# Kernel optimization log

Measured on AMD Instinct MI355X. Metric: run time of the kernel, lower is better.

The kernel has to match this reference:

```python
import jax, jax.numpy as jnp
import numpy as np

R, M, A = 512, 256, 256
B, L = 64, 4096


def setup_inputs() -> dict:
    key = jax.random.key(0)
    k1, k2, k3, k4, k5 = jax.random.split(key, 5)
    return {
        "hidden_state": jax.random.normal(k1, (B, R), dtype=jnp.float32),
        "feature_vectors": jax.random.normal(k2, (B, L, M), dtype=jnp.float32),
        "Wa": jax.random.normal(k3, (A, R), dtype=jnp.float32) / np.sqrt(R),
        "Ua": jax.random.normal(k4, (A, M), dtype=jnp.float32) / np.sqrt(M),
        "w": jax.random.normal(k5, (A, 1), dtype=jnp.float32),
        "ba": jnp.zeros((1, A), dtype=jnp.float32),
    }


def reference(hidden_state, feature_vectors, Wa, Ua, w, ba):
    # q: [B, A] broadcast over L; k: [B, L, A]
    q = hidden_state @ Wa.T + ba                      # [B, A]
    k = jnp.einsum("blm,am->bla", feature_vectors, Ua)  # [B, L, A]
    e = jnp.tanh(q[:, None, :] + k) @ w               # [B, L, 1]
    attn = jax.nn.softmax(e, axis=1)                  # softmax over L
    context = jnp.sum(attn * feature_vectors, axis=1)  # [B, M]
    return context
```

## Files before the change

kernel.cpp:

```cpp
#include <hip/hip_runtime.h>
#include <hip/hip_bf16.h>

#define B_  64
#define R_  512
#define M_  256
#define A_  256
#define L_  4096

typedef float    f32x4 __attribute__((ext_vector_type(4)));
typedef _Float16 f16x8 __attribute__((ext_vector_type(8)));

__global__ __launch_bounds__(256) void k_q(const float* __restrict__ h,
                                           const float* __restrict__ Wa,
                                           const float* __restrict__ ba,
                                           float* __restrict__ q) {
  int b = blockIdx.x;
  int tid = threadIdx.x;
  int wv = tid >> 6, lane = tid & 63;
  const f32x4* hp = (const f32x4*)(h + (size_t)b * R_ + lane * 8);
  f32x4 h0 = hp[0], h1 = hp[1];
#pragma unroll 4
  for (int i = 0; i < 64; ++i) {
    int a = wv * 64 + i;
    const f32x4* wp = (const f32x4*)(Wa + (size_t)a * R_ + lane * 8);
    f32x4 w0 = wp[0], w1 = wp[1];
    f32x4 pr = h0 * w0 + h1 * w1;
    float p = (pr.x + pr.y) + (pr.z + pr.w);
#pragma unroll
    for (int m = 1; m < 64; m <<= 1) p += __shfl_xor(p, m);
    if (lane == 0) q[b * A_ + a] = p + ba[a];
  }
}

__global__ __launch_bounds__(256) void k_e(const float* __restrict__ fv,
                                           const float* __restrict__ Ua,
                                           const float* __restrict__ q,
                                           const float* __restrict__ w,
                                           float* __restrict__ e) {
  __shared__ __align__(16) _Float16 sUa[64][264];
  __shared__ float sq[A_];
  __shared__ float sw[A_];
  int tid = threadIdx.x;
  int b  = blockIdx.x >> 5;
  int l0 = (blockIdx.x & 31) * 128;
  int wv = tid >> 6, lane = tid & 63;
  int quad = lane >> 4, l16 = lane & 15;

  sq[tid] = q[b * A_ + tid];
  sw[tid] = w[tid];

  f16x8 afrag[2][8];
#pragma unroll
  for (int rs = 0; rs < 2; ++rs) {
    const float* rowp = fv + ((size_t)b * L_ + (size_t)(l0 + wv * 32 + rs * 16 + l16)) * M_ + quad * 8;
#pragma unroll
    for (int s = 0; s < 8; ++s) {
      f32x4 x = *(const f32x4*)(rowp + s * 32);
      f32x4 y = *(const f32x4*)(rowp + s * 32 + 4);
      f16x8 f;
      f[0] = (_Float16)x.x; f[1] = (_Float16)x.y; f[2] = (_Float16)x.z; f[3] = (_Float16)x.w;
      f[4] = (_Float16)y.x; f[5] = (_Float16)y.y; f[6] = (_Float16)y.z; f[7] = (_Float16)y.w;
      afrag[rs][s] = f;
    }
  }

  float eacc[2][4] = {{0.f, 0.f, 0.f, 0.f}, {0.f, 0.f, 0.f, 0.f}};

  for (int c = 0; c < 4; ++c) {
    __syncthreads();
    {
      int row = tid >> 2, seg = tid & 3;
      const float* src = Ua + (size_t)(c * 64 + row) * M_ + seg * 64;
      _Float16* dst = &sUa[row][seg * 64];
#pragma unroll
      for (int j = 0; j < 16; ++j) {
        f32x4 v = *(const f32x4*)(src + j * 4);
        dst[j * 4 + 0] = (_Float16)v.x; dst[j * 4 + 1] = (_Float16)v.y;
        dst[j * 4 + 2] = (_Float16)v.z; dst[j * 4 + 3] = (_Float16)v.w;
      }
    }
    __syncthreads();

    f32x4 acc[2][4];
#pragma unroll
    for (int rs = 0; rs < 2; ++rs)
#pragma unroll
      for (int t = 0; t < 4; ++t) acc[rs][t] = 0.f;

#pragma unroll
    for (int s = 0; s < 8; ++s) {
#pragma unroll
      for (int t = 0; t < 4; ++t) {
        f16x8 bfrag = *(const f16x8*)(&sUa[t * 16 + l16][s * 32 + quad * 8]);
        acc[0][t] = __builtin_amdgcn_mfma_f32_16x16x32_f16(afrag[0][s], bfrag, acc[0][t], 0, 0, 0);
        acc[1][t] = __builtin_amdgcn_mfma_f32_16x16x32_f16(afrag[1][s], bfrag, acc[1][t], 0, 0, 0);
      }
    }

#pragma unroll
    for (int rs = 0; rs < 2; ++rs)
#pragma unroll
      for (int t = 0; t < 4; ++t) {
        int col = c * 64 + t * 16 + l16;
        float qc = sq[col], wc = sw[col];
#pragma unroll
        for (int i = 0; i < 4; ++i) {
          float x = qc + acc[rs][t][i];
          float ex = __expf(2.0f * x);
          float th = 1.0f - 2.0f * __builtin_amdgcn_rcpf(ex + 1.0f);
          eacc[rs][i] += th * wc;
        }
      }
  }

#pragma unroll
  for (int rs = 0; rs < 2; ++rs)
#pragma unroll
    for (int i = 0; i < 4; ++i) {
      float v = eacc[rs][i];
      v += __shfl_xor(v, 1); v += __shfl_xor(v, 2);
      v += __shfl_xor(v, 4); v += __shfl_xor(v, 8);
      if (l16 == 0)
        e[(size_t)b * L_ + l0 + wv * 32 + rs * 16 + quad * 4 + i] = v;
    }
}

__global__ __launch_bounds__(256) void k_softmax(const float* __restrict__ e,
                                                 float* __restrict__ attn) {
  __shared__ float red[8];
  int b = blockIdx.x, t = threadIdx.x;
  int wv = t >> 6, lane = t & 63;
  float v[16];
  float mx = -1e30f;
#pragma unroll
  for (int i = 0; i < 16; ++i) {
    v[i] = e[(size_t)b * L_ + i * 256 + t];
    mx = fmaxf(mx, v[i]);
  }
#pragma unroll
  for (int m = 1; m < 64; m <<= 1) mx = fmaxf(mx, __shfl_xor(mx, m));
  if (lane == 0) red[wv] = mx;
  __syncthreads();
  mx = fmaxf(fmaxf(red[0], red[1]), fmaxf(red[2], red[3]));
  float s = 0.f;
#pragma unroll
  for (int i = 0; i < 16; ++i) { v[i] = __expf(v[i] - mx); s += v[i]; }
#pragma unroll
  for (int m = 1; m < 64; m <<= 1) s += __shfl_xor(s, m);
  if (lane == 0) red[4 + wv] = s;
  __syncthreads();
  s = (red[4] + red[5]) + (red[6] + red[7]);
  float inv = 1.0f / s;
#pragma unroll
  for (int i = 0; i < 16; ++i) attn[(size_t)b * L_ + i * 256 + t] = v[i] * inv;
}

__global__ __launch_bounds__(256) void k_ctx(const float* __restrict__ fv,
                                             const float* __restrict__ attn,
                                             float* __restrict__ out) {
  __shared__ float sattn[256];
  __shared__ float part[4][256];
  int t = threadIdx.x;
  int b  = blockIdx.x >> 4;
  int l0 = (blockIdx.x & 15) * 256;
  int g = t >> 6, lane = t & 63;
  sattn[t] = attn[(size_t)b * L_ + l0 + t];
  __syncthreads();
  f32x4 acc = 0.f;
  const f32x4* base = (const f32x4*)(fv + ((size_t)b * L_ + l0) * M_) + lane;
#pragma unroll 4
  for (int l = g; l < 256; l += 4) {
    acc += sattn[l] * base[(size_t)l * (M_ / 4)];
  }
  ((f32x4*)part[g])[lane] = acc;
  __syncthreads();
  float sum = (part[0][t] + part[1][t]) + (part[2][t] + part[3][t]);
  atomicAdd(out + (size_t)b * M_ + t, sum);
}

extern "C" void kernel_launch(void* const* d_in, const int* in_sizes, int n_in,
                              void* d_out, int out_size, void* d_ws, size_t ws_size,
                              hipStream_t stream) {
  const float* h  = (const float*)d_in[0];
  const float* fv = (const float*)d_in[1];
  const float* Wa = (const float*)d_in[2];
  const float* Ua = (const float*)d_in[3];
  const float* w  = (const float*)d_in[4];
  const float* ba = (const float*)d_in[5];
  float* out = (float*)d_out;

  char* ws = (char*)d_ws;
  float* q    = (float*)ws;
  float* e    = (float*)(ws + (64 * 1024));
  float* attn = (float*)(ws + (64 * 1024) + (1024 * 1024));

  hipMemsetAsync(d_out, 0, (size_t)B_ * M_ * sizeof(float), stream);
  k_q<<<dim3(B_), dim3(256), 0, stream>>>(h, Wa, ba, q);
  k_e<<<dim3(B_ * (L_ / 128)), dim3(256), 0, stream>>>(fv, Ua, q, w, e);
  k_softmax<<<dim3(B_), dim3(256), 0, stream>>>(e, attn);
  k_ctx<<<dim3(B_ * 16), dim3(256), 0, stream>>>(fv, attn, out);
}
```

Baseline: 514.2 us.

## Fuse score, softmax and context into one flash-style kernel with split reduction

Merges the score, softmax and context kernels into a single pass. Each block computes its local max, exp-sum and weighted feature sum from the fp16 fragments already in registers, and a small final kernel rescales and combines the per-tile partials. Ua is converted to fp16 once in a prep kernel and its B fragments are read straight from global/L2 rather than staged through shared memory. This drops the second 256MB read of feature_vectors, the e/attn round trips and the memset, but the context sum now uses fp16-rounded features, which costs accuracy.

```diff
diff --git a/kernel.cpp b/kernel.cpp
--- a/kernel.cpp
+++ b/kernel.cpp
@@ -6,9 +6,21 @@
 #define M_  256
 #define A_  256
 #define L_  4096
+#define NT_ 32
+#define TR_ 128
 
 typedef float    f32x4 __attribute__((ext_vector_type(4)));
 typedef _Float16 f16x8 __attribute__((ext_vector_type(8)));
+
+__global__ __launch_bounds__(256) void k_prep(const float* __restrict__ Ua,
+                                              _Float16* __restrict__ Ua16) {
+  int idx = (blockIdx.x * 256 + threadIdx.x) * 4;
+  f32x4 v = *(const f32x4*)(Ua + idx);
+  Ua16[idx + 0] = (_Float16)v.x;
+  Ua16[idx + 1] = (_Float16)v.y;
+  Ua16[idx + 2] = (_Float16)v.z;
+  Ua16[idx + 3] = (_Float16)v.w;
+}
 
 __global__ __launch_bounds__(256) void k_q(const float* __restrict__ h,
                                            const float* __restrict__ Wa,
@@ -32,17 +44,21 @@
   }
 }
 
-__global__ __launch_bounds__(256) void k_e(const float* __restrict__ fv,
-                                           const float* __restrict__ Ua,
-                                           const float* __restrict__ q,
-                                           const float* __restrict__ w,
-                                           float* __restrict__ e) {
-  __shared__ __align__(16) _Float16 sUa[64][264];
+__global__ __launch_bounds__(256) void k_main(const float* __restrict__ fv,
+                                              const _Float16* __restrict__ Ua16,
+                                              const float* __restrict__ q,
+                                              const float* __restrict__ w,
+                                              float* __restrict__ blkmax,
+                                              float* __restrict__ blksum,
+                                              float* __restrict__ blkacc) {
   __shared__ float sq[A_];
   __shared__ float sw[A_];
+  __shared__ float sE[TR_];
+  __shared__ float sRed[8];
+  __shared__ float sAcc[4][M_];
   int tid = threadIdx.x;
   int b  = blockIdx.x >> 5;
-  int l0 = (blockIdx.x & 31) * 128;
+  int l0 = (blockIdx.x & 31) * TR_;
   int wv = tid >> 6, lane = tid & 63;
   int quad = lane >> 4, l16 = lane & 15;
 
@@ -63,54 +79,30 @@
       afrag[rs][s] = f;
     }
   }
+  __syncthreads();
 
   float eacc[2][4] = {{0.f, 0.f, 0.f, 0.f}, {0.f, 0.f, 0.f, 0.f}};
 
-  for (int c = 0; c < 4; ++c) {
-    __syncthreads();
-    {
-      int row = tid >> 2, seg = tid & 3;
-      const float* src = Ua + (size_t)(c * 64 + row) * M_ + seg * 64;
-      _Float16* dst = &sUa[row][seg * 64];
-#pragma unroll
-      for (int j = 0; j < 16; ++j) {
-        f32x4 v = *(const f32x4*)(src + j * 4);
-        dst[j * 4 + 0] = (_Float16)v.x; dst[j * 4 + 1] = (_Float16)v.y;
-        dst[j * 4 + 2] = (_Float16)v.z; dst[j * 4 + 3] = (_Float16)v.w;
-      }
-    }
-    __syncthreads();
-
-    f32x4 acc[2][4];
-#pragma unroll
-    for (int rs = 0; rs < 2; ++rs)
-#pragma unroll
-      for (int t = 0; t < 4; ++t) acc[rs][t] = 0.f;
-
+#pragma unroll 4
+  for (int t = 0; t < 16; ++t) {
+    f32x4 acc0 = 0.f, acc1 = 0.f;
+    const f16x8* bp = (const f16x8*)(Ua16 + ((size_t)(t * 16 + l16) << 8) + quad * 8);
 #pragma unroll
     for (int s = 0; s < 8; ++s) {
-#pragma unroll
-      for (int t = 0; t < 4; ++t) {
-        f16x8 bfrag = *(const f16x8*)(&sUa[t * 16 + l16][s * 32 + quad * 8]);
-        acc[0][t] = __builtin_amdgcn_mfma_f32_16x16x32_f16(afrag[0][s], bfrag, acc[0][t], 0, 0, 0);
-        acc[1][t] = __builtin_amdgcn_mfma_f32_16x16x32_f16(afrag[1][s], bfrag, acc[1][t], 0, 0, 0);
-      }
-    }
-
-#pragma unroll
-    for (int rs = 0; rs < 2; ++rs)
-#pragma unroll
-      for (int t = 0; t < 4; ++t) {
-        int col = c * 64 + t * 16 + l16;
-        float qc = sq[col], wc = sw[col];
-#pragma unroll
-        for (int i = 0; i < 4; ++i) {
-          float x = qc + acc[rs][t][i];
-          float ex = __expf(2.0f * x);
-          float th = 1.0f - 2.0f * __builtin_amdgcn_rcpf(ex + 1.0f);
-          eacc[rs][i] += th * wc;
-        }
-      }
+      f16x8 bf = bp[s * 4];
+      acc0 = __builtin_amdgcn_mfma_f32_16x16x32_f16(afrag[0][s], bf, acc0, 0, 0, 0);
+      acc1 = __builtin_amdgcn_mfma_f32_16x16x32_f16(afrag[1][s], bf, acc1, 0, 0, 0);
+    }
+    float qc = sq[t * 16 + l16], wc = sw[t * 16 + l16];
+#pragma unroll
+    for (int i = 0; i < 4; ++i) {
+      float x0 = qc + acc0[i];
+      float e0 = __expf(2.0f * x0);
+      eacc[0][i] += (1.0f - 2.0f * __builtin_amdgcn_rcpf(e0 + 1.0f)) * wc;
+      float x1 = qc + acc1[i];
+      float e1 = __expf(2.0f * x1);
+      eacc[1][i] += (1.0f - 2.0f * __builtin_amdgcn_rcpf(e1 + 1.0f)) * wc;
+    }
   }
 
 #pragma unroll
@@ -120,62 +112,70 @@
       float v = eacc[rs][i];
       v += __shfl_xor(v, 1); v += __shfl_xor(v, 2);
       v += __shfl_xor(v, 4); v += __shfl_xor(v, 8);
-      if (l16 == 0)
-        e[(size_t)b * L_ + l0 + wv * 32 + rs * 16 + quad * 4 + i] = v;
-    }
-}
-
-__global__ __launch_bounds__(256) void k_softmax(const float* __restrict__ e,
-                                                 float* __restrict__ attn) {
-  __shared__ float red[8];
+      if (l16 == 0) sE[wv * 32 + rs * 16 + quad * 4 + i] = v;
+    }
+  __syncthreads();
+
+  float m = (tid < TR_) ? sE[tid] : -1e30f;
+#pragma unroll
+  for (int k = 1; k < 64; k <<= 1) m = fmaxf(m, __shfl_xor(m, k));
+  if (lane == 0) sRed[wv] = m;
+  __syncthreads();
+  float mx = fmaxf(fmaxf(sRed[0], sRed[1]), fmaxf(sRed[2], sRed[3]));
+
+  float p0 = __expf(sE[wv * 32 + l16] - mx);
+  float p1 = __expf(sE[wv * 32 + 16 + l16] - mx);
+
+  float ps = (quad == 0) ? (p0 + p1) : 0.f;
+#pragma unroll
+  for (int k = 1; k < 64; k <<= 1) ps += __shfl_xor(ps, k);
+  if (lane == 0) sRed[4 + wv] = ps;
+
+#pragma unroll
+  for (int s = 0; s < 8; ++s) {
+    float c[8];
+#pragma unroll
+    for (int j = 0; j < 8; ++j)
+      c[j] = p0 * (float)afrag[0][s][j] + p1 * (float)afrag[1][s][j];
+#pragma unroll
+    for (int k = 1; k < 16; k <<= 1) {
+#pragma unroll
+      for (int j = 0; j < 8; ++j) c[j] += __shfl_xor(c[j], k);
+    }
+    if (l16 == 0) {
+#pragma unroll
+      for (int j = 0; j < 8; ++j) sAcc[wv][s * 32 + quad * 8 + j] = c[j];
+    }
+  }
+  __syncthreads();
+
+  float colsum = (sAcc[0][tid] + sAcc[1][tid]) + (sAcc[2][tid] + sAcc[3][tid]);
+  blkacc[(size_t)blockIdx.x * M_ + tid] = colsum;
+  if (tid == 0) {
+    blkmax[blockIdx.x] = mx;
+    blksum[blockIdx.x] = (sRed[4] + sRed[5]) + (sRed[6] + sRed[7]);
+  }
+}
+
+__global__ __launch_bounds__(256) void k_fin(const float* __restrict__ blkmax,
+                                             const float* __restrict__ blksum,
+                                             const float* __restrict__ blkacc,
+                                             float* __restrict__ out) {
+  __shared__ float sSc[NT_];
   int b = blockIdx.x, t = threadIdx.x;
-  int wv = t >> 6, lane = t & 63;
-  float v[16];
-  float mx = -1e30f;
-#pragma unroll
-  for (int i = 0; i < 16; ++i) {
-    v[i] = e[(size_t)b * L_ + i * 256 + t];
-    mx = fmaxf(mx, v[i]);
-  }
-#pragma unroll
-  for (int m = 1; m < 64; m <<= 1) mx = fmaxf(mx, __shfl_xor(mx, m));
-  if (lane == 0) red[wv] = mx;
-  __syncthreads();
-  mx = fmaxf(fmaxf(red[0], red[1]), fmaxf(red[2], red[3]));
-  float s = 0.f;
-#pragma unroll
-  for (int i = 0; i < 16; ++i) { v[i] = __expf(v[i] - mx); s += v[i]; }
-#pragma unroll
-  for (int m = 1; m < 64; m <<= 1) s += __shfl_xor(s, m);
-  if (lane == 0) red[4 + wv] = s;
-  __syncthreads();
-  s = (red[4] + red[5]) + (red[6] + red[7]);
-  float inv = 1.0f / s;
-#pragma unroll
-  for (int i = 0; i < 16; ++i) attn[(size_t)b * L_ + i * 256 + t] = v[i] * inv;
-}
-
-__global__ __launch_bounds__(256) void k_ctx(const float* __restrict__ fv,
-                                             const float* __restrict__ attn,
-                                             float* __restrict__ out) {
-  __shared__ float sattn[256];
-  __shared__ float part[4][256];
-  int t = threadIdx.x;
-  int b  = blockIdx.x >> 4;
-  int l0 = (blockIdx.x & 15) * 256;
-  int g = t >> 6, lane = t & 63;
-  sattn[t] = attn[(size_t)b * L_ + l0 + t];
-  __syncthreads();
-  f32x4 acc = 0.f;
-  const f32x4* base = (const f32x4*)(fv + ((size_t)b * L_ + l0) * M_) + lane;
+  float M = -1e30f;
+#pragma unroll
+  for (int i = 0; i < NT_; ++i) M = fmaxf(M, blkmax[b * NT_ + i]);
+  if (t < NT_) sSc[t] = __expf(blkmax[b * NT_ + t] - M);
+  __syncthreads();
+  float acc = 0.f, S = 0.f;
 #pragma unroll 4
-  for (int l = g; l < 256; l += 4) {
-    acc += sattn[l] * base[(size_t)l * (M_ / 4)];
-  }
-  ((f32x4*)part[g])[lane] = acc;
-  __syncthreads();
-  float sum = (part[0][t] + part[1][t]) + (part[2][t] + part[3][t]);
-  atomicAdd(out + (size_t)b * M_ + t, sum);
+  for (int i = 0; i < NT_; ++i) {
+    float sc = sSc[i];
+    S += blksum[b * NT_ + i] * sc;
+    acc += blkacc[(size_t)(b * NT_ + i) * M_ + t] * sc;
+  }
+  out[b * M_ + t] = acc / S;
 }
 
 extern "C" void kernel_launch(void* const* d_in, const int* in_sizes, int n_in,
@@ -190,13 +190,14 @@
   float* out = (float*)d_out;
 
   char* ws = (char*)d_ws;
-  float* q    = (float*)ws;
-  float* e    = (float*)(ws + (64 * 1024));
-  float* attn = (float*)(ws + (64 * 1024) + (1024 * 1024));
-
-  hipMemsetAsync(d_out, 0, (size_t)B_ * M_ * sizeof(float), stream);
+  float*    q      = (float*)(ws);
+  _Float16* Ua16   = (_Float16*)(ws + 65536);
+  float*    blkmax = (float*)(ws + 196608);
+  float*    blksum = (float*)(ws + 204800);
+  float*    blkacc = (float*)(ws + 212992);
+
+  k_prep<<<dim3(64), dim3(256), 0, stream>>>(Ua, Ua16);
   k_q<<<dim3(B_), dim3(256), 0, stream>>>(h, Wa, ba, q);
-  k_e<<<dim3(B_ * (L_ / 128)), dim3(256), 0, stream>>>(fv, Ua, q, w, e);
-  k_softmax<<<dim3(B_), dim3(256), 0, stream>>>(e, attn);
-  k_ctx<<<dim3(B_ * 16), dim3(256), 0, stream>>>(fv, attn, out);
-}
+  k_main<<<dim3(B_ * NT_), dim3(256), 0, stream>>>(fv, Ua16, q, w, blkmax, blksum, blkacc);
+  k_fin<<<dim3(B_), dim3(256), 0, stream>>>(blkmax, blksum, blkacc, out);
+}
```

Result: slower. 555.5 us (+8.0%).
